# Kernel optimization log

Measured on AMD Instinct MI355X. Metric: run time of the kernel, lower is better.

## Reference

```python
import jax, jax.numpy as jnp
import numpy as np

N_NODES = 100000
IN_CH = 128
HID = 128   # 2 * out_channels
OUT = 64    # out_channels
N_EDGES = 1000000


def _glorot(key, shape):
    lim = np.sqrt(6.0 / (shape[0] + shape[1]))
    return jax.random.uniform(key, shape, jnp.float32, -lim, lim)


def setup_inputs() -> dict:
    key = jax.random.key(0)
    ks = jax.random.split(key, 8)
    x = jax.random.normal(ks[0], (N_NODES, IN_CH), jnp.float32)
    edge_index = jax.random.randint(ks[1], (2, N_EDGES), 0, N_NODES, jnp.int64)
    return {
        "x": x,
        "edge_index": edge_index,
        # conv1: in -> 2*out
        "W1_l": _glorot(ks[2], (IN_CH, HID)),
        "W1_r": _glorot(ks[3], (IN_CH, HID)),
        "b1": jnp.zeros((HID,), jnp.float32),
        # conv_mu: 2*out -> out
        "Wmu_l": _glorot(ks[4], (HID, OUT)),
        "Wmu_r": _glorot(ks[5], (HID, OUT)),
        "bmu": jnp.zeros((OUT,), jnp.float32),
        # conv_logstd: 2*out -> out
        "Wls_l": _glorot(ks[6], (HID, OUT)),
        "Wls_r": _glorot(ks[7], (HID, OUT)),
        "bls": jnp.zeros((OUT,), jnp.float32),
    }


def _sage_conv(x, src, dst, W_l, W_r, b, n_nodes):
    # mean-aggregate neighbor features: messages flow src -> dst (PyG source_to_target)
    agg = jax.ops.segment_sum(x[src], dst, num_segments=n_nodes)          # [N, d]
    deg = jax.ops.segment_sum(jnp.ones(src.shape, x.dtype), dst, num_segments=n_nodes)
    agg = agg / jnp.maximum(deg, 1.0)[:, None]
    return agg @ W_l + x @ W_r + b


def reference(x, edge_index, W1_l, W1_r, b1, Wmu_l, Wmu_r, bmu, Wls_l, Wls_r, bls):
    src, dst = edge_index[0], edge_index[1]
    n = x.shape[0]
    h = jax.nn.relu(_sage_conv(x, src, dst, W1_l, W1_r, b1, n))
    mu = _sage_conv(h, src, dst, Wmu_l, Wmu_r, bmu, n)
    logstd = _sage_conv(h, src, dst, Wls_l, Wls_r, bls, n)
    return (mu, logstd)
```

## Files before the change

### kernel.cpp

```cpp
#include <hip/hip_runtime.h>

#define NN 100000
#define IC 128
#define OC 64
#define NE 1000000

#define NBUCK 64
#define BN 1568
#define RCAP 18432
#define EPB 2048
#define CAPA 64
#define GPAD 16
#define LDW 136
#define CVT_BLOCKS 6250

typedef __attribute__((ext_vector_type(8))) short short8;
typedef __attribute__((ext_vector_type(4))) float f32x4;

static __device__ __forceinline__ float b2f(unsigned short u) {
    unsigned v = ((unsigned)u) << 16;
    float f;
    __builtin_memcpy(&f, &v, 4);
    return f;
}
static __device__ __forceinline__ unsigned short f2b(float f) {
    unsigned u;
    __builtin_memcpy(&u, &f, 4);
    u += 0x7fff + ((u >> 16) & 1);
    return (unsigned short)(u >> 16);
}

__global__ __launch_bounds__(256) void k_binA(const int* __restrict__ src,
                                              const int* __restrict__ dst,
                                              int* __restrict__ gcur,
                                              unsigned* __restrict__ bins) {
    __shared__ unsigned buf[NBUCK][CAPA];
    __shared__ int lcnt[NBUCK];
    const int t = threadIdx.x;
    if (t < NBUCK) lcnt[t] = 0;
    __syncthreads();
    const int e0 = blockIdx.x * EPB;
#pragma unroll
    for (int q = 0; q < EPB / 256; ++q) {
        int e = e0 + q * 256 + t;
        if (e < NE) {
            int d = dst[e];
            int s = src[e];
            int b = d / BN;
            unsigned packed = ((unsigned)(d - b * BN) << 17) | (unsigned)s;
            int idx = atomicAdd(&lcnt[b], 1);
            if (idx < CAPA) {
                buf[b][idx] = packed;
            } else {
                int g = atomicAdd(&gcur[b * GPAD], 1);
                if (g < RCAP) bins[(size_t)b * RCAP + g] = packed;
            }
        }
    }
    __syncthreads();
    const int wid = t >> 6, lane = t & 63;
    for (int b = wid * 16; b < wid * 16 + 16; ++b) {
        int c = lcnt[b];
        if (c > CAPA) c = CAPA;
        if (c > 0) {
            int g = 0;
            if (lane == 0) g = atomicAdd(&gcur[b * GPAD], c);
            g = __shfl(g, 0, 64);
            if (lane < c && g + lane < RCAP)
                bins[(size_t)b * RCAP + g + lane] = buf[b][lane];
        }
    }
}

__global__ __launch_bounds__(512) void k_binB(const int* __restrict__ gcur,
                                              const unsigned* __restrict__ bins,
                                              int* __restrict__ row_ptr,
                                              int* __restrict__ csr) {
    __shared__ int lc[2048];
    __shared__ int rk[2048];
    __shared__ int tsum[512];
    __shared__ int seg[RCAP];
    __shared__ int sh_bs;
    const int b = blockIdx.x;
    const int t = threadIdx.x;
    const int base = b * BN;
    const int nloc = (NN - base < BN) ? (NN - base) : BN;
    if (t < 64) {
        int v = gcur[t * GPAD];
        if (v > RCAP) v = RCAP;
        int s = v;
        for (int off = 1; off < 64; off <<= 1) {
            int u = __shfl_up(s, off, 64);
            if (t >= off) s += u;
        }
        if (t == b) sh_bs = s - v;
        if (b == 0 && t == 63) row_ptr[NN] = s;
    }
    for (int i = t; i < 2048; i += 512) { lc[i] = 0; rk[i] = 0; }
    __syncthreads();
    int c = gcur[b * GPAD];
    if (c > RCAP) c = RCAP;
    const unsigned* mb = bins + (size_t)b * RCAP;
    for (int i = t; i < c; i += 512) atomicAdd(&lc[mb[i] >> 17], 1);
    __syncthreads();
    int loc[4], s = 0;
#pragma unroll
    for (int q = 0; q < 4; ++q) { loc[q] = lc[t * 4 + q]; s += loc[q]; }
    tsum[t] = s;
    __syncthreads();
    for (int off = 1; off < 512; off <<= 1) {
        int u = (t >= off) ? tsum[t - off] : 0;
        __syncthreads();
        tsum[t] += u;
        __syncthreads();
    }
    int run = tsum[t] - s;
#pragma unroll
    for (int q = 0; q < 4; ++q) { lc[t * 4 + q] = run; run += loc[q]; }
    __syncthreads();
    const int bs = sh_bs;
    for (int i = t; i < nloc; i += 512) row_ptr[base + i] = bs + lc[i];
    for (int i = t; i < c; i += 512) {
        unsigned p = mb[i];
        int dl = p >> 17;
        int r = atomicAdd(&rk[dl], 1);
        seg[lc[dl] + r] = (int)(p & 0x1FFFFu);
    }
    __syncthreads();
    for (int i = t; i < c; i += 512) csr[bs + i] = seg[i];
}

__global__ __launch_bounds__(256) void k_prep(
    const float* __restrict__ x, unsigned short* __restrict__ xb,
    const float* __restrict__ W1l, const float* __restrict__ W1r,
    const float* __restrict__ Wml, const float* __restrict__ Wmr,
    const float* __restrict__ Wsl, const float* __restrict__ Wsr,
    unsigned short* __restrict__ Wf1, unsigned short* __restrict__ Wf2) {
    const int blk = blockIdx.x;
    if (blk < CVT_BLOCKS) {
        int t = blk * 256 + threadIdx.x;
        const float4* p = (const float4*)x + (size_t)t * 2;
        float4 f0 = p[0], f1 = p[1];
        short8 o;
        o[0] = (short)f2b(f0.x); o[1] = (short)f2b(f0.y);
        o[2] = (short)f2b(f0.z); o[3] = (short)f2b(f0.w);
        o[4] = (short)f2b(f1.x); o[5] = (short)f2b(f1.y);
        o[6] = (short)f2b(f1.z); o[7] = (short)f2b(f1.w);
        *((short8*)xb + t) = o;
    } else {
        int t = (blk - CVT_BLOCKS) * 256 + threadIdx.x;
        if (t >= 2 * 4096) return;
        const int layer = t >> 12;
        const int f = t & 4095;
        const int lane = f & 63;
        const int nt = (f >> 6) & 7;
        const int ks = f >> 9;
        const int col = nt * 16 + (lane & 15);
        const int kb = ks * 32 + ((lane >> 4) << 3);
        short8 o;
#pragma unroll
        for (int e = 0; e < 8; ++e) {
            const int k = kb + e;
            float v;
            if (layer == 0) {
                v = (k < 128) ? W1l[k * 128 + col] : W1r[(k - 128) * 128 + col];
            } else {
                if (col < OC) v = (k < 128) ? Wml[k * OC + col] : Wmr[(k - 128) * OC + col];
                else {
                    int c2 = col - OC;
                    v = (k < 128) ? Wsl[k * OC + c2] : Wsr[(k - 128) * OC + c2];
                }
            }
            o[e] = (short)f2b(v);
        }
        unsigned short* W = (layer == 0) ? Wf1 : Wf2;
        *(short8*)(W + (size_t)f * 8) = o;
    }
}

__global__ __launch_bounds__(256) void k_agg(const unsigned short* __restrict__ feat,
                                             const int* __restrict__ row_ptr,
                                             const int* __restrict__ csr,
                                             unsigned short* __restrict__ agg) {
    const int lane = threadIdx.x & 63;
    const int wid = threadIdx.x >> 6;
    const int slot = lane >> 4;
    const int cg = lane & 15;
    const int node = blockIdx.x * 16 + wid * 4 + slot;
    if (node >= NN) return;
    const int beg = row_ptr[node];
    const int end = row_ptr[node + 1];
    float acc[8];
#pragma unroll
    for (int q = 0; q < 8; ++q) acc[q] = 0.f;

    for (int j = beg; j < end; j += 8) {
        const int nl = end - j;
        short8 v[8];
#pragma unroll
        for (int u = 0; u < 8; ++u) {
            if (u < nl) {
                int s = csr[j + u];
                v[u] = *(const short8*)(feat + (size_t)s * IC + cg * 8);
            }
        }
#pragma unroll
        for (int u = 0; u < 8; ++u) {
            if (u < nl) {
#pragma unroll
                for (int q = 0; q < 8; ++q) acc[q] += b2f((unsigned short)v[u][q]);
            }
        }
    }
    float inv = 1.0f / fmaxf((float)(end - beg), 1.0f);
    short8 o;
#pragma unroll
    for (int q = 0; q < 8; ++q) o[q] = (short)f2b(acc[q] * inv);
    *(short8*)(agg + (size_t)node * IC + cg * 8) = o;
}

template <int MODE>
__global__ __launch_bounds__(256) void k_gemm(
    const unsigned short* __restrict__ Agg, const unsigned short* __restrict__ Xb,
    const unsigned short* __restrict__ Wf,
    const float* __restrict__ bias0, const float* __restrict__ bias1,
    unsigned short* __restrict__ hout, float* __restrict__ out_mu,
    float* __restrict__ out_ls) {
    const int lane = threadIdx.x & 63;
    const int wid = threadIdx.x >> 6;
    const int rowg = blockIdx.x * 128 + wid * 32;
    const int r16 = lane & 15;
    const int k8 = (lane >> 4) * 8;

    __shared__ unsigned short smem[MODE == 0 ? (4 * 32 * LDW) : 16384];
    short8* bsm = (short8*)smem;

    int rA[2];
#pragma unroll
    for (int m = 0; m < 2; ++m) {
        int r = rowg + m * 16 + r16;
        rA[m] = (r < NN) ? r : (NN - 1);
    }

    short8 aF[2][8];
#pragma unroll
    for (int ks = 0; ks < 4; ++ks) {
        aF[0][ks] = *(const short8*)(Agg + (size_t)rA[0] * IC + ks * 32 + k8);
        aF[1][ks] = *(const short8*)(Agg + (size_t)rA[1] * IC + ks * 32 + k8);
    }
#pragma unroll
    for (int ks = 0; ks < 4; ++ks) {
        aF[0][4 + ks] = *(const short8*)(Xb + (size_t)rA[0] * IC + ks * 32 + k8);
        aF[1][4 + ks] = *(const short8*)(Xb + (size_t)rA[1] * IC + ks * 32 + k8);
    }

    const short8* Wg = (const short8*)Wf;
#pragma unroll
    for (int i = 0; i < 8; ++i)
        bsm[i * 256 + threadIdx.x] = Wg[i * 256 + threadIdx.x];

#pragma unroll
    for (int ks = 0; ks < 8; ++ks)
        asm volatile("" :: "v"(aF[0][ks]), "v"(aF[1][ks]));

    __syncthreads();

    f32x4 acc[2][8];
#pragma unroll
    for (int m = 0; m < 2; ++m)
#pragma unroll
        for (int nt = 0; nt < 8; ++nt) acc[m][nt] = (f32x4){0.f, 0.f, 0.f, 0.f};

#pragma unroll
    for (int ks = 0; ks < 4; ++ks) {
        short8 bF[8];
#pragma unroll
        for (int nt = 0; nt < 8; ++nt) bF[nt] = bsm[(ks * 8 + nt) * 64 + lane];
#pragma unroll
        for (int nt = 0; nt < 8; ++nt) {
            acc[0][nt] = __builtin_amdgcn_mfma_f32_16x16x32_bf16(aF[0][ks], bF[nt], acc[0][nt], 0, 0, 0);
            acc[1][nt] = __builtin_amdgcn_mfma_f32_16x16x32_bf16(aF[1][ks], bF[nt], acc[1][nt], 0, 0, 0);
        }
    }
    __syncthreads();
#pragma unroll
    for (int i = 0; i < 8; ++i)
        bsm[i * 256 + threadIdx.x] = Wg[2048 + i * 256 + threadIdx.x];
    __syncthreads();
#pragma unroll
    for (int ks = 4; ks < 8; ++ks) {
        short8 bF[8];
#pragma unroll
        for (int nt = 0; nt < 8; ++nt) bF[nt] = bsm[((ks - 4) * 8 + nt) * 64 + lane];
#pragma unroll
        for (int nt = 0; nt < 8; ++nt) {
            acc[0][nt] = __builtin_amdgcn_mfma_f32_16x16x32_bf16(aF[0][ks], bF[nt], acc[0][nt], 0, 0, 0);
            acc[1][nt] = __builtin_amdgcn_mfma_f32_16x16x32_bf16(aF[1][ks], bF[nt], acc[1][nt], 0, 0, 0);
        }
    }

    const int rbase = (lane >> 4) * 4;
    if (MODE == 0) {
        __syncthreads();
        unsigned short* ws = smem + wid * 32 * LDW;
#pragma unroll
        for (int m = 0; m < 2; ++m) {
#pragma unroll
            for (int nt = 0; nt < 8; ++nt) {
                const int c = nt * 16 + r16;
                const float bv = bias0[c];
#pragma unroll
                for (int q = 0; q < 4; ++q) {
                    float v = fmaxf(acc[m][nt][q] + bv, 0.f);
                    ws[(m * 16 + rbase + q) * LDW + c] = f2b(v);
                }
            }
        }
        __syncthreads();
#pragma unroll
        for (int p = 0; p < 8; ++p) {
            const int rloc = p * 4 + (lane >> 4);
            const int row = rowg + rloc;
            if (row < NN) {
                short8 v = *(const short8*)&ws[rloc * LDW + r16 * 8];
                *(short8*)(hout + (size_t)row * IC + r16 * 8) = v;
            }
        }
    } else {
#pragma unroll
        for (int m = 0; m < 2; ++m) {
#pragma unroll
            for (int nt = 0; nt < 8; ++nt) {
                const int c = nt * 16 + r16;
                const float bv = (c < OC) ? bias0[c] : bias1[c - OC];
#pragma unroll
                for (int q = 0; q < 4; ++q) {
                    const int row = rowg + m * 16 + rbase + q;
                    if (row >= NN) continue;
                    float v = acc[m][nt][q] + bv;
                    if (c < OC) out_mu[(size_t)row * OC + c] = v;
                    else        out_ls[(size_t)row * OC + (c - OC)] = v;
                }
            }
        }
    }
}

extern "C" void kernel_launch(void* const* d_in, const int* in_sizes, int n_in,
                              void* d_out, int out_size, void* d_ws, size_t ws_size,
                              hipStream_t stream) {
    const float* x   = (const float*)d_in[0];
    const int*   ei  = (const int*)d_in[1];
    const float* W1l = (const float*)d_in[2];
    const float* W1r = (const float*)d_in[3];
    const float* b1  = (const float*)d_in[4];
    const float* Wml = (const float*)d_in[5];
    const float* Wmr = (const float*)d_in[6];
    const float* bm  = (const float*)d_in[7];
    const float* Wsl = (const float*)d_in[8];
    const float* Wsr = (const float*)d_in[9];
    const float* bs  = (const float*)d_in[10];

    const int* src = ei;
    const int* dst = ei + NE;

    char* w = (char*)d_ws;
    unsigned short* xb   = (unsigned short*)(w);
    unsigned short* hb   = (unsigned short*)(w + 25600000);
    unsigned short* aggb = (unsigned short*)(w + 51200000);
    unsigned short* Wf1  = (unsigned short*)(w + 76800000);
    unsigned short* Wf2  = (unsigned short*)(w + 76865536);
    int* row_ptr  = (int*)(w + 76931072);
    int* csr      = (int*)(w + 77331136);
    int* gcur     = (int*)(w + 81331136);
    unsigned* bins = (unsigned*)(w + 81336256);

    float* out_mu = (float*)d_out;
    float* out_ls = out_mu + (size_t)NN * OC;

    const int gemm_grid = (NN + 127) / 128;
    const int agg_grid = (NN + 15) / 16;
    const int binA_grid = (NE + EPB - 1) / EPB;

    hipMemsetAsync(gcur, 0, NBUCK * GPAD * sizeof(int), stream);
    k_binA<<<binA_grid, 256, 0, stream>>>(src, dst, gcur, bins);
    k_binB<<<NBUCK, 512, 0, stream>>>(gcur, bins, row_ptr, csr);

    k_prep<<<CVT_BLOCKS + 32, 256, 0, stream>>>(x, xb, W1l, W1r, Wml, Wmr, Wsl, Wsr, Wf1, Wf2);

    k_agg<<<agg_grid, 256, 0, stream>>>(xb, row_ptr, csr, aggb);
    k_gemm<0><<<gemm_grid, 256, 0, stream>>>(aggb, xb, Wf1, b1, nullptr,
                                             hb, nullptr, nullptr);

    k_agg<<<agg_grid, 256, 0, stream>>>(hb, row_ptr, csr, aggb);
    k_gemm<1><<<gemm_grid, 256, 0, stream>>>(aggb, hb, Wf2, bm, bs,
                                             nullptr, out_mu, out_ls);
}
```

Baseline: 198.5 us.

## Gather layer-1 neighbors in FP8, fuse binning with prep, use finer buckets

Quantizes x to FP8 alongside the bf16 conversion, and the first aggregation gathers 8-byte FP8 rows instead of 16-byte bf16 rows. This halves the random-gather traffic of that layer. The edge-binning pass is fused into the same launch as the x/weight conversion, and the bucket count goes from 64 to 256 with smaller buckets, so the CSR-build kernel gets more parallel blocks. The cost is FP8 precision loss in the first-layer mean aggregation, and a smaller per-block shared capacity that may spill more edges to global atomics.

```diff
diff --git a/kernel.cpp b/kernel.cpp
--- a/kernel.cpp
+++ b/kernel.cpp
@@ -5,13 +5,14 @@
 #define OC 64
 #define NE 1000000
 
-#define NBUCK 64
-#define BN 1568
-#define RCAP 18432
+#define NBUCK 256
+#define BN 392
+#define RCAP 4608
 #define EPB 2048
-#define CAPA 64
+#define CAPA 24
 #define GPAD 16
 #define LDW 136
+#define BINA_GRID 489
 #define CVT_BLOCKS 6250
 
 typedef __attribute__((ext_vector_type(8))) short short8;
@@ -30,16 +31,55 @@
     return (unsigned short)(u >> 16);
 }
 
-__global__ __launch_bounds__(256) void k_binA(const int* __restrict__ src,
-                                              const int* __restrict__ dst,
-                                              int* __restrict__ gcur,
-                                              unsigned* __restrict__ bins) {
-    __shared__ unsigned buf[NBUCK][CAPA];
-    __shared__ int lcnt[NBUCK];
-    const int t = threadIdx.x;
-    if (t < NBUCK) lcnt[t] = 0;
-    __syncthreads();
-    const int e0 = blockIdx.x * EPB;
+#if defined(__has_builtin)
+#if __has_builtin(__builtin_amdgcn_cvt_pk_fp8_f32) && __has_builtin(__builtin_amdgcn_cvt_pk_f32_fp8)
+#define HW_FP8 1
+#endif
+#endif
+
+static __device__ __forceinline__ unsigned f2q1(float f) {
+    unsigned u;
+    __builtin_memcpy(&u, &f, 4);
+    unsigned s = (u >> 24) & 0x80u;
+    unsigned a = u & 0x7FFFFFFFu;
+    if (a < 0x3C000000u) return s;
+    if (a < 0x3C800000u) return s | 0x08u;
+    if (a >= 0x43E00000u) return s | 0x7Eu;
+    a += 0x7FFFFu + ((a >> 20) & 1u);
+    unsigned e = (a >> 23) - 120u;
+    unsigned m = (a >> 20) & 7u;
+    unsigned c = (e << 3) | m;
+    if (c > 0x7Eu) c = 0x7Eu;
+    return s | c;
+}
+static __device__ __forceinline__ float q1f(unsigned q) {
+    unsigned em = q & 0x7Fu;
+    unsigned s = (q & 0x80u) << 24;
+    unsigned u = (em >= 8u) ? (s | (((em >> 3) + 120u) << 23) | ((em & 7u) << 20)) : s;
+    float f;
+    __builtin_memcpy(&f, &u, 4);
+    return f;
+}
+
+static __device__ __forceinline__ unsigned pack4_fp8(float a, float b, float c, float d) {
+#ifdef HW_FP8
+    int r = __builtin_amdgcn_cvt_pk_fp8_f32(a, b, 0, false);
+    r = __builtin_amdgcn_cvt_pk_fp8_f32(c, d, r, true);
+    return (unsigned)r;
+#else
+    return f2q1(a) | (f2q1(b) << 8) | (f2q1(c) << 16) | (f2q1(d) << 24);
+#endif
+}
+
+__device__ __forceinline__ void binA_body(int blk, int t,
+                                          const int* __restrict__ src,
+                                          const int* __restrict__ dst,
+                                          int* __restrict__ gcur,
+                                          unsigned* __restrict__ bins,
+                                          unsigned (*buf)[CAPA], int* lcnt, int* goff) {
+    lcnt[t] = 0;
+    __syncthreads();
+    const int e0 = blk * EPB;
 #pragma unroll
     for (int q = 0; q < EPB / 256; ++q) {
         int e = e0 + q * 256 + t;
@@ -58,87 +98,39 @@
         }
     }
     __syncthreads();
+    int c = lcnt[t];
+    if (c > CAPA) c = CAPA;
+    if (c > 0) goff[t] = atomicAdd(&gcur[t * GPAD], c);
+    __syncthreads();
     const int wid = t >> 6, lane = t & 63;
-    for (int b = wid * 16; b < wid * 16 + 16; ++b) {
-        int c = lcnt[b];
-        if (c > CAPA) c = CAPA;
-        if (c > 0) {
-            int g = 0;
-            if (lane == 0) g = atomicAdd(&gcur[b * GPAD], c);
-            g = __shfl(g, 0, 64);
-            if (lane < c && g + lane < RCAP)
-                bins[(size_t)b * RCAP + g + lane] = buf[b][lane];
-        }
-    }
-}
-
-__global__ __launch_bounds__(512) void k_binB(const int* __restrict__ gcur,
-                                              const unsigned* __restrict__ bins,
-                                              int* __restrict__ row_ptr,
-                                              int* __restrict__ csr) {
-    __shared__ int lc[2048];
-    __shared__ int rk[2048];
-    __shared__ int tsum[512];
-    __shared__ int seg[RCAP];
-    __shared__ int sh_bs;
-    const int b = blockIdx.x;
-    const int t = threadIdx.x;
-    const int base = b * BN;
-    const int nloc = (NN - base < BN) ? (NN - base) : BN;
-    if (t < 64) {
-        int v = gcur[t * GPAD];
-        if (v > RCAP) v = RCAP;
-        int s = v;
-        for (int off = 1; off < 64; off <<= 1) {
-            int u = __shfl_up(s, off, 64);
-            if (t >= off) s += u;
-        }
-        if (t == b) sh_bs = s - v;
-        if (b == 0 && t == 63) row_ptr[NN] = s;
-    }
-    for (int i = t; i < 2048; i += 512) { lc[i] = 0; rk[i] = 0; }
-    __syncthreads();
-    int c = gcur[b * GPAD];
-    if (c > RCAP) c = RCAP;
-    const unsigned* mb = bins + (size_t)b * RCAP;
-    for (int i = t; i < c; i += 512) atomicAdd(&lc[mb[i] >> 17], 1);
-    __syncthreads();
-    int loc[4], s = 0;
-#pragma unroll
-    for (int q = 0; q < 4; ++q) { loc[q] = lc[t * 4 + q]; s += loc[q]; }
-    tsum[t] = s;
-    __syncthreads();
-    for (int off = 1; off < 512; off <<= 1) {
-        int u = (t >= off) ? tsum[t - off] : 0;
-        __syncthreads();
-        tsum[t] += u;
-        __syncthreads();
-    }
-    int run = tsum[t] - s;
-#pragma unroll
-    for (int q = 0; q < 4; ++q) { lc[t * 4 + q] = run; run += loc[q]; }
-    __syncthreads();
-    const int bs = sh_bs;
-    for (int i = t; i < nloc; i += 512) row_ptr[base + i] = bs + lc[i];
-    for (int i = t; i < c; i += 512) {
-        unsigned p = mb[i];
-        int dl = p >> 17;
-        int r = atomicAdd(&rk[dl], 1);
-        seg[lc[dl] + r] = (int)(p & 0x1FFFFu);
-    }
-    __syncthreads();
-    for (int i = t; i < c; i += 512) csr[bs + i] = seg[i];
-}
-
-__global__ __launch_bounds__(256) void k_prep(
+    for (int b = wid * 64; b < wid * 64 + 64; ++b) {
+        int cb = lcnt[b];
+        if (cb > CAPA) cb = CAPA;
+        if (lane < cb) {
+            int g = goff[b] + lane;
+            if (g < RCAP) bins[(size_t)b * RCAP + g] = buf[b][lane];
+        }
+    }
+}
+
+__global__ __launch_bounds__(256) void k_front(
+    const int* __restrict__ src, const int* __restrict__ dst,
+    int* __restrict__ gcur, unsigned* __restrict__ bins,
     const float* __restrict__ x, unsigned short* __restrict__ xb,
+    unsigned char* __restrict__ xq,
     const float* __restrict__ W1l, const float* __restrict__ W1r,
     const float* __restrict__ Wml, const float* __restrict__ Wmr,
     const float* __restrict__ Wsl, const float* __restrict__ Wsr,
     unsigned short* __restrict__ Wf1, unsigned short* __restrict__ Wf2) {
+    __shared__ unsigned buf[NBUCK][CAPA];
+    __shared__ int lcnt[NBUCK];
+    __shared__ int goff[NBUCK];
     const int blk = blockIdx.x;
-    if (blk < CVT_BLOCKS) {
-        int t = blk * 256 + threadIdx.x;
+    const int tid = threadIdx.x;
+    if (blk < BINA_GRID) {
+        binA_body(blk, tid, src, dst, gcur, bins, buf, lcnt, goff);
+    } else if (blk < BINA_GRID + CVT_BLOCKS) {
+        int t = (blk - BINA_GRID) * 256 + tid;
         const float4* p = (const float4*)x + (size_t)t * 2;
         float4 f0 = p[0], f1 = p[1];
         short8 o;
@@ -147,8 +139,12 @@
         o[4] = (short)f2b(f1.x); o[5] = (short)f2b(f1.y);
         o[6] = (short)f2b(f1.z); o[7] = (short)f2b(f1.w);
         *((short8*)xb + t) = o;
+        uint2 q;
+        q.x = pack4_fp8(f0.x, f0.y, f0.z, f0.w);
+        q.y = pack4_fp8(f1.x, f1.y, f1.z, f1.w);
+        *((uint2*)xq + t) = q;
     } else {
-        int t = (blk - CVT_BLOCKS) * 256 + threadIdx.x;
+        int t = (blk - BINA_GRID - CVT_BLOCKS) * 256 + tid;
         if (t >= 2 * 4096) return;
         const int layer = t >> 12;
         const int f = t & 4095;
@@ -178,7 +174,68 @@
     }
 }
 
+__global__ __launch_bounds__(256) void k_binB(const int* __restrict__ gcur,
+                                              const unsigned* __restrict__ bins,
+                                              int* __restrict__ row_ptr,
+                                              int* __restrict__ csr) {
+    __shared__ int lc[512];
+    __shared__ int rk[512];
+    __shared__ int tsum[256];
+    __shared__ int seg[RCAP];
+    __shared__ int sh_bs;
+    const int b = blockIdx.x;
+    const int t = threadIdx.x;
+    const int base = b * BN;
+    const int nloc = (NN - base < BN) ? (NN - base) : BN;
+    int v = gcur[t * GPAD];
+    if (v > RCAP) v = RCAP;
+    tsum[t] = v;
+    __syncthreads();
+    for (int off = 1; off < 256; off <<= 1) {
+        int u = (t >= off) ? tsum[t - off] : 0;
+        __syncthreads();
+        tsum[t] += u;
+        __syncthreads();
+    }
+    if (t == b) sh_bs = tsum[t] - v;
+    if (b == 0 && t == 255) row_ptr[NN] = tsum[255];
+    lc[t] = 0; lc[t + 256] = 0;
+    rk[t] = 0; rk[t + 256] = 0;
+    __syncthreads();
+    int c = gcur[b * GPAD];
+    if (c > RCAP) c = RCAP;
+    const unsigned* mb = bins + (size_t)b * RCAP;
+    for (int i = t; i < c; i += 256) atomicAdd(&lc[mb[i] >> 17], 1);
+    __syncthreads();
+    int l0 = lc[2 * t], l1 = lc[2 * t + 1];
+    int s = l0 + l1;
+    tsum[t] = s;
+    __syncthreads();
+    for (int off = 1; off < 256; off <<= 1) {
+        int u = (t >= off) ? tsum[t - off] : 0;
+        __syncthreads();
+        tsum[t] += u;
+        __syncthreads();
+    }
+    int run = tsum[t] - s;
+    lc[2 * t] = run;
+    lc[2 * t + 1] = run + l0;
+    __syncthreads();
+    const int bs = sh_bs;
+    for (int i = t; i < nloc; i += 256) row_ptr[base + i] = bs + lc[i];
+    for (int i = t; i < c; i += 256) {
+        unsigned p = mb[i];
+        int dl = p >> 17;
+        int r = atomicAdd(&rk[dl], 1);
+        seg[lc[dl] + r] = (int)(p & 0x1FFFFu);
+    }
+    __syncthreads();
+    for (int i = t; i < c; i += 256) csr[bs + i] = seg[i];
+}
+
+template <int FP8>
 __global__ __launch_bounds__(256) void k_agg(const unsigned short* __restrict__ feat,
+                                             const unsigned char* __restrict__ featq,
                                              const int* __restrict__ row_ptr,
                                              const int* __restrict__ csr,
                                              unsigned short* __restrict__ agg) {
@@ -194,21 +251,55 @@
 #pragma unroll
     for (int q = 0; q < 8; ++q) acc[q] = 0.f;
 
-    for (int j = beg; j < end; j += 8) {
-        const int nl = end - j;
-        short8 v[8];
-#pragma unroll
-        for (int u = 0; u < 8; ++u) {
-            if (u < nl) {
-                int s = csr[j + u];
-                v[u] = *(const short8*)(feat + (size_t)s * IC + cg * 8);
-            }
-        }
-#pragma unroll
-        for (int u = 0; u < 8; ++u) {
-            if (u < nl) {
-#pragma unroll
-                for (int q = 0; q < 8; ++q) acc[q] += b2f((unsigned short)v[u][q]);
+    if (FP8) {
+        for (int j = beg; j < end; j += 8) {
+            const int nl = end - j;
+            uint2 v[8];
+#pragma unroll
+            for (int u = 0; u < 8; ++u) {
+                if (u < nl) {
+                    int s = csr[j + u];
+                    v[u] = *(const uint2*)(featq + (size_t)s * IC + cg * 8);
+                }
+            }
+#pragma unroll
+            for (int u = 0; u < 8; ++u) {
+                if (u < nl) {
+#ifdef HW_FP8
+                    auto p0 = __builtin_amdgcn_cvt_pk_f32_fp8((int)v[u].x, false);
+                    auto p1 = __builtin_amdgcn_cvt_pk_f32_fp8((int)v[u].x, true);
+                    auto p2 = __builtin_amdgcn_cvt_pk_f32_fp8((int)v[u].y, false);
+                    auto p3 = __builtin_amdgcn_cvt_pk_f32_fp8((int)v[u].y, true);
+                    acc[0] += p0[0]; acc[1] += p0[1];
+                    acc[2] += p1[0]; acc[3] += p1[1];
+                    acc[4] += p2[0]; acc[5] += p2[1];
+                    acc[6] += p3[0]; acc[7] += p3[1];
+#else
+#pragma unroll
+                    for (int q = 0; q < 4; ++q) acc[q] += q1f((v[u].x >> (8 * q)) & 0xFFu);
+#pragma unroll
+                    for (int q = 0; q < 4; ++q) acc[4 + q] += q1f((v[u].y >> (8 * q)) & 0xFFu);
+#endif
+                }
+            }
+        }
+    } else {
+        for (int j = beg; j < end; j += 8) {
+            const int nl = end - j;
+            short8 v[8];
+#pragma unroll
+            for (int u = 0; u < 8; ++u) {
+                if (u < nl) {
+                    int s = csr[j + u];
+                    v[u] = *(const short8*)(feat + (size_t)s * IC + cg * 8);
+                }
+            }
+#pragma unroll
+            for (int u = 0; u < 8; ++u) {
+                if (u < nl) {
+#pragma unroll
+                    for (int q = 0; q < 8; ++q) acc[q] += b2f((unsigned short)v[u][q]);
+                }
             }
         }
     }
@@ -371,28 +462,27 @@
     unsigned short* Wf1  = (unsigned short*)(w + 76800000);
     unsigned short* Wf2  = (unsigned short*)(w + 76865536);
     int* row_ptr  = (int*)(w + 76931072);
-    int* csr      = (int*)(w + 77331136);
-    int* gcur     = (int*)(w + 81331136);
-    unsigned* bins = (unsigned*)(w + 81336256);
+    int* csr      = (int*)(w + 77331200);
+    int* gcur     = (int*)(w + 81331200);
+    unsigned* bins = (unsigned*)(w + 81347584);
+    unsigned char* xq = (unsigned char*)(w + 86066176);
 
     float* out_mu = (float*)d_out;
     float* out_ls = out_mu + (size_t)NN * OC;
 
     const int gemm_grid = (NN + 127) / 128;
     const int agg_grid = (NN + 15) / 16;
-    const int binA_grid = (NE + EPB - 1) / EPB;
 
     hipMemsetAsync(gcur, 0, NBUCK * GPAD * sizeof(int), stream);
-    k_binA<<<binA_grid, 256, 0, stream>>>(src, dst, gcur, bins);
-    k_binB<<<NBUCK, 512, 0, stream>>>(gcur, bins, row_ptr, csr);
-
-    k_prep<<<CVT_BLOCKS + 32, 256, 0, stream>>>(x, xb, W1l, W1r, Wml, Wmr, Wsl, Wsr, Wf1, Wf2);
-
-    k_agg<<<agg_grid, 256, 0, stream>>>(xb, row_ptr, csr, aggb);
+    k_front<<<BINA_GRID + CVT_BLOCKS + 32, 256, 0, stream>>>(
+        src, dst, gcur, bins, x, xb, xq, W1l, W1r, Wml, Wmr, Wsl, Wsr, Wf1, Wf2);
+    k_binB<<<NBUCK, 256, 0, stream>>>(gcur, bins, row_ptr, csr);
+
+    k_agg<1><<<agg_grid, 256, 0, stream>>>(nullptr, xq, row_ptr, csr, aggb);
     k_gemm<0><<<gemm_grid, 256, 0, stream>>>(aggb, xb, Wf1, b1, nullptr,
                                              hb, nullptr, nullptr);
 
-    k_agg<<<agg_grid, 256, 0, stream>>>(hb, row_ptr, csr, aggb);
+    k_agg<0><<<agg_grid, 256, 0, stream>>>(hb, nullptr, row_ptr, csr, aggb);
     k_gemm<1><<<gemm_grid, 256, 0, stream>>>(aggb, hb, Wf2, bm, bs,
                                              nullptr, out_mu, out_ls);
 }
```

Result: faster. 174.1 us (-12.3%).
